# Kernel optimization log

Hardware: AMD Instinct MI355X
Metric: run time of the kernel (lower is better)

The kernel has to match this reference:

```python
import jax, jax.numpy as jnp
import numpy as np

DIM = 1024
NH = 16        # query heads
NKV = 4        # kv heads
HD = 64        # head dim
GROUPS = NH // NKV
SPATIAL = 16
NZ = SPATIAL * SPATIAL  # 256 latent tokens with 2D structure
SOFT_CAP = 50.0
SCALE = HD ** -0.5
EPS = 1e-6


def rope_2d_cos_sin(nz, hd, spatial, dtype):
    # 2D RoPE: first half of head_dim encodes row position, second half column.
    pos = jnp.arange(nz)
    row = (pos // spatial).astype(jnp.float32)
    col = (pos % spatial).astype(jnp.float32)
    quarter = hd // 4
    inv_freq = 1.0 / (10000.0 ** (jnp.arange(quarter, dtype=jnp.float32) / quarter))
    f_row = row[:, None] * inv_freq[None, :]   # (nz, hd/4)
    f_col = col[:, None] * inv_freq[None, :]   # (nz, hd/4)
    emb = jnp.concatenate([f_row, f_col], axis=-1)      # (nz, hd/2)
    emb = jnp.concatenate([emb, emb], axis=-1)          # (nz, hd)
    return jnp.cos(emb).astype(dtype), jnp.sin(emb).astype(dtype)


def rotate_half(x):
    x1, x2 = jnp.split(x, 2, axis=-1)
    return jnp.concatenate([-x2, x1], axis=-1)


def apply_rotary(x, cos, sin):
    return x * cos + rotate_half(x) * sin


def rms_norm(x, w):
    # RMSNorm over head_dim with learned per-dim scale (QKNorm)
    return x * jax.lax.rsqrt(jnp.mean(x * x, axis=-1, keepdims=True) + EPS) * w


def setup_inputs() -> dict:
    key = jax.random.key(0)
    ks = jax.random.split(key, 7)
    B, T, S = 4, 16, 264
    x = jax.random.normal(ks[0], (B, T, S, DIM), dtype=jnp.float32)
    wq = jax.random.normal(ks[1], (NH * HD, DIM), dtype=jnp.float32) * 0.02
    wk = jax.random.normal(ks[2], (NKV * HD, DIM), dtype=jnp.float32) * 0.02
    wv = jax.random.normal(ks[3], (NKV * HD, DIM), dtype=jnp.float32) * 0.02
    wo = jax.random.normal(ks[4], (DIM, NH * HD), dtype=jnp.float32) * 0.02
    q_norm_w = jnp.ones((HD,), dtype=jnp.float32)
    k_norm_w = jnp.ones((HD,), dtype=jnp.float32)
    return {"x": x, "wq": wq, "wk": wk, "wv": wv, "wo": wo,
            "q_norm_w": q_norm_w, "k_norm_w": k_norm_w}


def reference(x, wq, wk, wv, wo, q_norm_w, k_norm_w):
    B, T, S, D = x.shape
    xf = x.reshape(B * T, S, D)
    # projections (torch Linear: y = x @ W.T)
    q = (xf @ wq.T).reshape(B * T, S, NH, HD).transpose(0, 2, 1, 3)   # (BT,NH,S,HD)
    k = (xf @ wk.T).reshape(B * T, S, NKV, HD).transpose(0, 2, 1, 3)  # (BT,NKV,S,HD)
    v = (xf @ wv.T).reshape(B * T, S, NKV, HD).transpose(0, 2, 1, 3)
    # QKNorm
    q = rms_norm(q, q_norm_w)
    k = rms_norm(k, k_norm_w)
    # partial 2D RoPE on latent tokens only
    cos, sin = rope_2d_cos_sin(NZ, HD, SPATIAL, q.dtype)
    cos = cos[None, None]  # (1,1,NZ,HD)
    sin = sin[None, None]
    q = jnp.concatenate([apply_rotary(q[:, :, :NZ], cos, sin), q[:, :, NZ:]], axis=2)
    k = jnp.concatenate([apply_rotary(k[:, :, :NZ], cos, sin), k[:, :, NZ:]], axis=2)
    # GQA: expand kv heads (repeat_interleave == jnp.repeat)
    k = jnp.repeat(k, GROUPS, axis=1)
    v = jnp.repeat(v, GROUPS, axis=1)
    # attention with soft cap
    attn = jnp.einsum("bhqd,bhkd->bhqk", q, k) * SCALE
    attn = SOFT_CAP * jnp.tanh(attn / SOFT_CAP)
    attn = jax.nn.softmax(attn, axis=-1)
    out = jnp.einsum("bhqk,bhkd->bhqd", attn, v)
    out = out.transpose(0, 2, 1, 3).reshape(B * T, S, NH * HD)
    out = out @ wo.T
    return out.reshape(B, T, S, D)
```

## Files before the change

### kernel.cpp

```cpp
#include <hip/hip_runtime.h>

typedef __bf16 bf16;
typedef __bf16 bf16x8 __attribute__((ext_vector_type(8)));
typedef float  f32x4  __attribute__((ext_vector_type(4)));

#define DIM   1024
#define NH    16
#define NKV   4
#define HD    64
#define SLEN  264
#define BTOT  64
#define MROWS (BTOT * SLEN)
#define NQKV  1536
#define NZ    256
#define VPAD  288

__device__ __forceinline__ void gl_lds16(const bf16* g, bf16* l) {
    __builtin_amdgcn_global_load_lds((__attribute__((address_space(1))) void*)(g),
                                     (__attribute__((address_space(3))) void*)(l),
                                     16, 0, 0);
}

__global__ void cvt_f32_bf16(const float* __restrict__ src, bf16* __restrict__ dst, int n) {
    int i = (blockIdx.x * 256 + threadIdx.x) * 4;
    if (i < n) {
        float4 v = *(const float4*)(src + i);
        dst[i + 0] = (bf16)v.x; dst[i + 1] = (bf16)v.y;
        dst[i + 2] = (bf16)v.z; dst[i + 3] = (bf16)v.w;
    }
}

__global__ void cvt_wcat(const float* __restrict__ wq, const float* __restrict__ wk,
                         const float* __restrict__ wv, bf16* __restrict__ dst) {
    int i = (blockIdx.x * 256 + threadIdx.x) * 4;
    const float* src; int off;
    if (i < 1024 * 1024)      { src = wq; off = i; }
    else if (i < 1280 * 1024) { src = wk; off = i - 1024 * 1024; }
    else                      { src = wv; off = i - 1280 * 1024; }
    float4 v = *(const float4*)(src + off);
    dst[i + 0] = (bf16)v.x; dst[i + 1] = (bf16)v.y;
    dst[i + 2] = (bf16)v.z; dst[i + 3] = (bf16)v.w;
}

__global__ void rope_tab_kernel(float2* __restrict__ ctab) {
    int i = blockIdx.x * 256 + threadIdx.x;
    int s = i >> 5, d = i & 31;
    const float LN1 = 0.5756462732485115f;
    float pos = (d < 16) ? (float)(s >> 4) : (float)(s & 15);
    float ang = pos * expf(-(float)(d & 15) * LN1);
    float sn, cs; sincosf(ang, &sn, &cs);
    ctab[i] = make_float2(cs, sn);
}


#define GATE4  asm volatile("s_waitcnt vmcnt(4)" ::: "memory")
#define NOGATE do {} while (0)

#define STAGE_A(DST, H, KT) do {                                                       \
    gl_lds16(Ag + (size_t)((H) * 128 + ars[0]) * DIM + (KT) * 64 + acs[0] * 8,         \
             (DST) + (wid * 64) * 8);                                                  \
    gl_lds16(Ag + (size_t)((H) * 128 + ars[1]) * DIM + (KT) * 64 + acs[1] * 8,         \
             (DST) + (512 + wid * 64) * 8);                                            \
} while (0)

#define STAGE_B(DST, KS, KT) do {                                                      \
    gl_lds16(Bg + (size_t)brs[0] * DIM + (KT) * 64 + (KS) * 32 + bcs[0] * 8,           \
             (DST) + (wid * 64) * 8);                                                  \
    gl_lds16(Bg + (size_t)brs[1] * DIM + (KT) * 64 + (KS) * 32 + bcs[1] * 8,           \
             (DST) + (512 + wid * 64) * 8);                                            \
} while (0)

#define PHASE(AARR, BARR, AA, KS, STAGE_STMT, GATE_STMT) do {                          \
    const bf16* Ab_ = (AARR) + aRdBase + axor[KS];                                     \
    const bf16* Bb_ = (BARR) + bRdBase + bxorv;                                        \
    bf16x8 af_[4], bf_[4];                                                             \
    _Pragma("unroll")                                                                  \
    for (int i_ = 0; i_ < 4; i_++) af_[i_] = *(const bf16x8*)(Ab_ + i_ * 1024);        \
    _Pragma("unroll")                                                                  \
    for (int n_ = 0; n_ < 4; n_++) bf_[n_] = *(const bf16x8*)(Bb_ + n_ * 512);         \
    STAGE_STMT;                                                                        \
    GATE_STMT;                                                                         \
    asm volatile("s_barrier" ::: "memory");                                            \
    __builtin_amdgcn_s_setprio(1);                                                     \
    _Pragma("unroll")                                                                  \
    for (int i_ = 0; i_ < 4; i_++)                                                     \
        _Pragma("unroll")                                                              \
        for (int n_ = 0; n_ < 4; n_++)                                                 \
            acc[AA][i_][n_] = __builtin_amdgcn_mfma_f32_16x16x32_bf16(                 \
                af_[i_], bf_[n_], acc[AA][i_][n_], 0, 0, 0);                           \
    __builtin_amdgcn_s_setprio(0);                                                     \
    asm volatile("s_barrier" ::: "memory");                                            \
} while (0)

__device__ __forceinline__ void gemm256_core(const bf16* __restrict__ Ag,
                                             const bf16* __restrict__ Bg,
                                             f32x4 (&acc)[2][4][4]) {
    __shared__ __align__(16) bf16 A00[128 * 64], A01[128 * 64], A10[128 * 64], A11[128 * 64];
    __shared__ __align__(16) bf16 B00[256 * 32], B01[256 * 32], B10[256 * 32], B11[256 * 32];

    const int tid  = threadIdx.x;
    const int wid  = tid >> 6, lane = tid & 63;
    const int quad = lane >> 4, r16 = lane & 15;
    const int wm = wid & 1, wn = wid >> 1;

    int ars[2], acs[2], brs[2], bcs[2];
#pragma unroll
    for (int k = 0; k < 2; k++) {
        int s = k * 512 + tid;
        ars[k] = s >> 3; acs[k] = (s & 7) ^ (ars[k] & 7);
        brs[k] = s >> 2; bcs[k] = (s & 3) ^ (brs[k] & 3);
    }
    const int aRdBase = (wm * 64 + r16) * 64;
    const int bRdBase = (wn * 64 + r16) * 32;
    const int axor[2] = { (quad ^ (r16 & 7)) * 8, ((4 + quad) ^ (r16 & 7)) * 8 };
    const int bxorv   = (quad ^ (r16 & 3)) * 8;

    STAGE_A(A00, 0, 0); STAGE_A(A01, 1, 0);
    STAGE_B(B00, 0, 0); STAGE_B(B01, 1, 0);
    STAGE_A(A10, 0, 1); STAGE_B(B10, 0, 1);
    GATE4;
    asm volatile("s_barrier" ::: "memory");

#pragma unroll 1
    for (int it = 0; it < 8; ++it) {
        const int t1 = 2 * it + 1;
        int t2 = 2 * it + 2; if (t2 > 15) t2 = 15;
        int t3 = 2 * it + 3; if (t3 > 15) t3 = 15;
        PHASE(A00, B00, 0, 0, STAGE_A(A11, 1, t1), NOGATE);
        PHASE(A00, B01, 0, 1, STAGE_B(B11, 1, t1), NOGATE);
        PHASE(A01, B00, 1, 0, STAGE_A(A00, 0, t2), NOGATE);
        PHASE(A01, B01, 1, 1, STAGE_B(B00, 0, t2), GATE4);
        PHASE(A10, B10, 0, 0, STAGE_A(A01, 1, t2), NOGATE);
        PHASE(A10, B11, 0, 1, STAGE_B(B01, 1, t2), NOGATE);
        PHASE(A11, B10, 1, 0, STAGE_A(A10, 0, t3), NOGATE);
        PHASE(A11, B11, 1, 1, STAGE_B(B10, 0, t3), GATE4);
    }
}

__device__ __forceinline__ int xcd_swizzle(int orig, int nwg) {
    int q = nwg >> 3, r = nwg & 7;
    int xcd = orig & 7, lid = orig >> 3;
    return (xcd < r ? xcd * (q + 1) : r * (q + 1) + (xcd - r) * q) + lid;
}

__global__ __launch_bounds__(512) void gemm_qkv(const bf16* __restrict__ A,
                                                const bf16* __restrict__ Bw,
                                                bf16* __restrict__ out,
                                                const float* __restrict__ qw,
                                                const float* __restrict__ kw,
                                                const float2* __restrict__ ctab) {
    const int nwg = (MROWS / 256) * (NQKV / 256);
    int wg = xcd_swizzle(blockIdx.x, nwg);
    const int bm = wg / 6, bn = wg - bm * 6;

    f32x4 acc[2][4][4];
#pragma unroll
    for (int a = 0; a < 2; a++)
#pragma unroll
        for (int i = 0; i < 4; i++)
#pragma unroll
            for (int n = 0; n < 4; n++) acc[a][i][n] = (f32x4){0.f, 0.f, 0.f, 0.f};

    gemm256_core(A + (size_t)bm * 256 * DIM, Bw + (size_t)bn * 256 * DIM, acc);

    const int tid  = threadIdx.x;
    const int wid  = tid >> 6, lane = tid & 63;
    const int quad = lane >> 4, r16 = lane & 15;
    const int wm = wid & 1, wn = wid >> 1;
    const int colbase = bn * 256 + wn * 64;
    const int rowb    = bm * 256 + wm * 64;

    if (bn < 5) {
        const float* w = (bn < 4) ? qw : kw;
        float wreg[4];
#pragma unroll
        for (int n = 0; n < 4; n++) wreg[n] = w[n * 16 + r16];
#pragma unroll
        for (int a = 0; a < 2; a++)
#pragma unroll
            for (int i = 0; i < 4; i++)
#pragma unroll
                for (int r = 0; r < 4; r++) {
                    float ss = 0.f;
#pragma unroll
                    for (int n = 0; n < 4; n++) ss += acc[a][i][n][r] * acc[a][i][n][r];
                    ss += __shfl_xor(ss, 1, 64);
                    ss += __shfl_xor(ss, 2, 64);
                    ss += __shfl_xor(ss, 4, 64);
                    ss += __shfl_xor(ss, 8, 64);
                    float rms = rsqrtf(ss * (1.f / 64.f) + 1e-6f);
                    float xv[4];
#pragma unroll
                    for (int n = 0; n < 4; n++) xv[n] = acc[a][i][n][r] * rms * wreg[n];
                    int gm = rowb + a * 128 + i * 16 + quad * 4 + r;
                    int s = gm % SLEN;
                    if (s < NZ) {
                        float2 cs0 = ctab[s * 32 + r16];
                        float2 cs1 = ctab[s * 32 + 16 + r16];
                        float a0 = xv[0] * cs0.x - xv[2] * cs0.y;
                        float a2 = xv[2] * cs0.x + xv[0] * cs0.y;
                        float a1 = xv[1] * cs1.x - xv[3] * cs1.y;
                        float a3 = xv[3] * cs1.x + xv[1] * cs1.y;
                        xv[0] = a0; xv[1] = a1; xv[2] = a2; xv[3] = a3;
                    }
                    size_t rowoff = (size_t)gm * NQKV + colbase + r16;
#pragma unroll
                    for (int n = 0; n < 4; n++) out[rowoff + n * 16] = (bf16)xv[n];
                }
    } else {
#pragma unroll
        for (int a = 0; a < 2; a++)
#pragma unroll
            for (int i = 0; i < 4; i++)
#pragma unroll
                for (int r = 0; r < 4; r++) {
                    int gm = rowb + a * 128 + i * 16 + quad * 4 + r;
                    size_t rowoff = (size_t)gm * NQKV + colbase + r16;
#pragma unroll
                    for (int n = 0; n < 4; n++) out[rowoff + n * 16] = (bf16)acc[a][i][n][r];
                }
    }
}

__global__ __launch_bounds__(512) void gemm_bt(const bf16* __restrict__ A,
                                               const bf16* __restrict__ Bw,
                                               float* __restrict__ Cout) {
    const int nwg = (MROWS / 256) * (DIM / 256);
    int wg = xcd_swizzle(blockIdx.x, nwg);
    const int bm = wg / 4, bn = wg - bm * 4;

    f32x4 acc[2][4][4];
#pragma unroll
    for (int a = 0; a < 2; a++)
#pragma unroll
        for (int i = 0; i < 4; i++)
#pragma unroll
            for (int n = 0; n < 4; n++) acc[a][i][n] = (f32x4){0.f, 0.f, 0.f, 0.f};

    gemm256_core(A + (size_t)bm * 256 * DIM, Bw + (size_t)bn * 256 * DIM, acc);

    const int tid  = threadIdx.x;
    const int wid  = tid >> 6, lane = tid & 63;
    const int quad = lane >> 4, r16 = lane & 15;
    const int wm = wid & 1, wn = wid >> 1;
    const int colbase = bn * 256 + wn * 64;
    const int rowb    = bm * 256 + wm * 64;
#pragma unroll
    for (int a = 0; a < 2; a++)
#pragma unroll
        for (int i = 0; i < 4; i++)
#pragma unroll
            for (int r = 0; r < 4; r++) {
                int gm = rowb + a * 128 + i * 16 + quad * 4 + r;
                size_t rowoff = (size_t)gm * DIM + colbase + r16;
#pragma unroll
                for (int n = 0; n < 4; n++) Cout[rowoff + n * 16] = acc[a][i][n][r];
            }
}

__global__ __launch_bounds__(256) void vtrans_kernel(const bf16* __restrict__ qkv,
                                                     bf16* __restrict__ vt) {
    __shared__ bf16 Ls[64 * 272];
    const int tid = threadIdx.x;
    const int b = blockIdx.x, bt = b >> 2, kv = b & 3;
    const int part = tid >> 5;
    const int rr   = tid & 31;
#pragma unroll
    for (int pass = 0; pass < 9; ++pass) {
        int row = pass * 32 + rr;
        if (row < SLEN) {
            bf16x8 v = *(const bf16x8*)(qkv + (size_t)(bt * SLEN + row) * NQKV + 1280 + kv * 64 + part * 8);
#pragma unroll
            for (int j = 0; j < 8; j++) Ls[(part * 8 + j) * 272 + row] = v[j];
        }
    }
    __syncthreads();
    const int d = tid >> 2, seg = tid & 3;
    size_t obase = ((size_t)b * 64 + d) * VPAD;
#pragma unroll
    for (int m = 0; m < 9; ++m) {
        int col = seg * 72 + m * 8;
        bf16x8 o;
#pragma unroll
        for (int j = 0; j < 8; j++) {
            int s = col + j;
            o[j] = (s < SLEN) ? Ls[d * 272 + s] : (bf16)0.f;
        }
        *(bf16x8*)(vt + obase + col) = o;
    }
}

__global__ __launch_bounds__(256) void attn_kernel(const bf16* __restrict__ qkv,
                                                   const bf16* __restrict__ vt,
                                                   bf16* __restrict__ aout) {
    const int PLD = 40;
    __shared__ __align__(16) bf16 Pb[4][2][16 * PLD];

    const int tid = threadIdx.x;
    const int wid = tid >> 6, lane = tid & 63;
    const int quad = lane >> 4, r16 = lane & 15;
    const int qp = blockIdx.x;
    const int kv = blockIdx.y, bt = blockIdx.z;
    const int h = kv * 4 + wid;

    bf16x8 qa[2][2];
#pragma unroll
    for (int qi = 0; qi < 2; qi++) {
        int q0 = qp * 32 + qi * 16 + r16;
        int qcl = q0 < SLEN ? q0 : SLEN - 1;
        const bf16* qb = qkv + (size_t)(bt * SLEN + qcl) * NQKV + h * HD + quad * 8;
        qa[qi][0] = *(const bf16x8*)qb;
        qa[qi][1] = *(const bf16x8*)(qb + 32);
    }

    f32x4 oacc[2][4];
    float lsum[2][4];
#pragma unroll
    for (int qi = 0; qi < 2; qi++)
#pragma unroll
        for (int i = 0; i < 4; i++) { oacc[qi][i] = (f32x4){0.f, 0.f, 0.f, 0.f}; lsum[qi][i] = 0.f; }

    const bf16* kbase = qkv + (size_t)bt * SLEN * NQKV + 1024 + kv * HD + quad * 8;
    const bf16* vbase = vt + (size_t)(bt * 4 + kv) * HD * VPAD;

    bf16x8 nk[2][2];
#pragma unroll
    for (int kt = 0; kt < 2; kt++) {
        int key = kt * 16 + r16;
        const bf16* kp = kbase + (size_t)key * NQKV;
        nk[kt][0] = *(const bf16x8*)kp;
        nk[kt][1] = *(const bf16x8*)(kp + 32);
    }

    for (int c = 0; c < 9; ++c) {
        bf16x8 ck[2][2];
#pragma unroll
        for (int kt = 0; kt < 2; kt++) { ck[kt][0] = nk[kt][0]; ck[kt][1] = nk[kt][1]; }
        if (c < 8) {
#pragma unroll
            for (int kt = 0; kt < 2; kt++) {
                int key = (c + 1) * 32 + kt * 16 + r16;
                int kc = key < SLEN ? key : SLEN - 1;
                const bf16* kp = kbase + (size_t)kc * NQKV;
                nk[kt][0] = *(const bf16x8*)kp;
                nk[kt][1] = *(const bf16x8*)(kp + 32);
            }
        }
        bf16x8 cv[4];
#pragma unroll
        for (int dt = 0; dt < 4; ++dt)
            cv[dt] = *(const bf16x8*)(vbase + (size_t)(dt * 16 + r16) * VPAD + c * 32 + quad * 8);

        f32x4 s[2][2];
#pragma unroll
        for (int qi = 0; qi < 2; qi++)
#pragma unroll
            for (int kt = 0; kt < 2; kt++) {
                f32x4 t = (f32x4){0.f, 0.f, 0.f, 0.f};
                t = __builtin_amdgcn_mfma_f32_16x16x32_bf16(qa[qi][0], ck[kt][0], t, 0, 0, 0);
                t = __builtin_amdgcn_mfma_f32_16x16x32_bf16(qa[qi][1], ck[kt][1], t, 0, 0, 0);
                s[qi][kt] = t;
            }

#pragma unroll
        for (int qi = 0; qi < 2; qi++) {
            bf16* Pw = &Pb[wid][qi][0];
#pragma unroll
            for (int kt = 0; kt < 2; kt++)
#pragma unroll
                for (int r = 0; r < 4; ++r) {
                    int key = c * 32 + kt * 16 + r16;
                    float sc = s[qi][kt][r];
                    float z = sc * 0.0025f;
                    float z2 = z * z;
                    float poly = fmaf(z2, fmaf(z2, 0.133333333f, -0.333333333f), 1.f);
                    float p = exp2f(sc * 0.18033688f * poly);
                    p = (key < SLEN) ? p : 0.f;
                    bf16 pb = (bf16)p;
                    lsum[qi][r] += (float)pb;
                    Pw[(quad * 4 + r) * PLD + kt * 16 + r16] = pb;
                }
            bf16x8 pa = *(const bf16x8*)&Pw[r16 * PLD + quad * 8];
#pragma unroll
            for (int dt = 0; dt < 4; ++dt)
                oacc[qi][dt] = __builtin_amdgcn_mfma_f32_16x16x32_bf16(pa, cv[dt], oacc[qi][dt], 0, 0, 0);
        }
    }

#pragma unroll
    for (int qi = 0; qi < 2; qi++)
#pragma unroll
        for (int r = 0; r < 4; ++r) {
            float l = lsum[qi][r];
            l += __shfl_xor(l, 1, 64);
            l += __shfl_xor(l, 2, 64);
            l += __shfl_xor(l, 4, 64);
            l += __shfl_xor(l, 8, 64);
            float inv = 1.f / l;
            int q = qp * 32 + qi * 16 + quad * 4 + r;
            if (q < SLEN) {
                size_t base = (size_t)(bt * SLEN + q) * (NH * HD) + h * HD;
#pragma unroll
                for (int dt = 0; dt < 4; ++dt)
                    aout[base + dt * 16 + r16] = (bf16)(oacc[qi][dt][r] * inv);
            }
        }
}

extern "C" void kernel_launch(void* const* d_in, const int* in_sizes, int n_in,
                              void* d_out, int out_size, void* d_ws, size_t ws_size,
                              hipStream_t stream) {
    const float* x   = (const float*)d_in[0];
    const float* wq  = (const float*)d_in[1];
    const float* wk  = (const float*)d_in[2];
    const float* wv  = (const float*)d_in[3];
    const float* wo  = (const float*)d_in[4];
    const float* qnw = (const float*)d_in[5];
    const float* knw = (const float*)d_in[6];

    bf16* xbf  = (bf16*)d_ws;
    bf16* wcat = xbf  + (size_t)MROWS * DIM;
    bf16* wobf = wcat + (size_t)NQKV * DIM;
    bf16* qkv  = wobf + (size_t)DIM * DIM;
    bf16* vt   = qkv  + (size_t)MROWS * NQKV;
    float2* ctab = (float2*)(vt + (size_t)BTOT * NKV * HD * VPAD);
    bf16* aout = xbf;

    rope_tab_kernel<<<32, 256, 0, stream>>>(ctab);
    cvt_f32_bf16<<<(MROWS * DIM) / 1024, 256, 0, stream>>>(x, xbf, MROWS * DIM);
    cvt_wcat<<<(NQKV * DIM) / 1024, 256, 0, stream>>>(wq, wk, wv, wcat);
    cvt_f32_bf16<<<(DIM * DIM) / 1024, 256, 0, stream>>>(wo, wobf, DIM * DIM);

    gemm_qkv<<<(MROWS / 256) * (NQKV / 256), 512, 0, stream>>>(xbf, wcat, qkv, qnw, knw, ctab);
    vtrans_kernel<<<BTOT * NKV, 256, 0, stream>>>(qkv, vt);
    attn_kernel<<<dim3(9, NKV, BTOT), 256, 0, stream>>>(qkv, vt, aout);
    gemm_bt<<<(MROWS / 256) * (DIM / 256), 512, 0, stream>>>(aout, wobf, (float*)d_out);
}
```

Before: 372.0 us.

## Restructure QKV GEMM main loop to 32-wide K steps with double-buffered LDS

Rewrites the 256x256 GEMM core so each K step covers 32 columns instead of 64. The shared-memory layout becomes two A and two B buffers with a pair-row XOR swizzle, and the loop runs 16 iterations of 4 phases, each with finer-grained vmcnt(1) gating. Explicit lgkmcnt waits and sched_barriers are added so MFMA issue follows the LDS reads. The aim is finer overlap of global-to-LDS staging with MFMA work and smaller LDS use, at the cost of more barriers per unit of K.

```diff
diff --git a/kernel.cpp b/kernel.cpp
--- a/kernel.cpp
+++ b/kernel.cpp
@@ -52,95 +52,97 @@
     ctab[i] = make_float2(cs, sn);
 }
 
-
-#define GATE4  asm volatile("s_waitcnt vmcnt(4)" ::: "memory")
+__device__ __forceinline__ int xcd_swizzle(int orig, int nwg) {
+    int q = nwg >> 3, r = nwg & 7;
+    int xcd = orig & 7, lid = orig >> 3;
+    return (xcd < r ? xcd * (q + 1) : r * (q + 1) + (xcd - r) * q) + lid;
+}
+
+
+#define GATE1  asm volatile("s_waitcnt vmcnt(1)" ::: "memory")
 #define NOGATE do {} while (0)
 
-#define STAGE_A(DST, H, KT) do {                                                       \
-    gl_lds16(Ag + (size_t)((H) * 128 + ars[0]) * DIM + (KT) * 64 + acs[0] * 8,         \
-             (DST) + (wid * 64) * 8);                                                  \
-    gl_lds16(Ag + (size_t)((H) * 128 + ars[1]) * DIM + (KT) * 64 + acs[1] * 8,         \
-             (DST) + (512 + wid * 64) * 8);                                            \
-} while (0)
-
-#define STAGE_B(DST, KS, KT) do {                                                      \
-    gl_lds16(Bg + (size_t)brs[0] * DIM + (KT) * 64 + (KS) * 32 + bcs[0] * 8,           \
-             (DST) + (wid * 64) * 8);                                                  \
-    gl_lds16(Bg + (size_t)brs[1] * DIM + (KT) * 64 + (KS) * 32 + bcs[1] * 8,           \
-             (DST) + (512 + wid * 64) * 8);                                            \
-} while (0)
-
-#define PHASE(AARR, BARR, AA, KS, STAGE_STMT, GATE_STMT) do {                          \
-    const bf16* Ab_ = (AARR) + aRdBase + axor[KS];                                     \
-    const bf16* Bb_ = (BARR) + bRdBase + bxorv;                                        \
-    bf16x8 af_[4], bf_[4];                                                             \
-    _Pragma("unroll")                                                                  \
-    for (int i_ = 0; i_ < 4; i_++) af_[i_] = *(const bf16x8*)(Ab_ + i_ * 1024);        \
-    _Pragma("unroll")                                                                  \
-    for (int n_ = 0; n_ < 4; n_++) bf_[n_] = *(const bf16x8*)(Bb_ + n_ * 512);         \
-    STAGE_STMT;                                                                        \
-    GATE_STMT;                                                                         \
-    asm volatile("s_barrier" ::: "memory");                                            \
-    __builtin_amdgcn_s_setprio(1);                                                     \
-    _Pragma("unroll")                                                                  \
-    for (int i_ = 0; i_ < 4; i_++)                                                     \
-        _Pragma("unroll")                                                              \
-        for (int n_ = 0; n_ < 4; n_++)                                                 \
-            acc[AA][i_][n_] = __builtin_amdgcn_mfma_f32_16x16x32_bf16(                 \
-                af_[i_], bf_[n_], acc[AA][i_][n_], 0, 0, 0);                           \
-    __builtin_amdgcn_s_setprio(0);                                                     \
-    asm volatile("s_barrier" ::: "memory");                                            \
+#define STA(DBUF, SITE, KT) gl_lds16(Asrc[SITE] + (KT) * 32, (DBUF) + (SITE) * 4096 + wid * 512)
+#define STB(DBUF, SITE, KT) gl_lds16(Bsrc[SITE] + (KT) * 32, (DBUF) + (SITE) * 4096 + wid * 512)
+
+#define PHASE(Ad, Bd, AA, GATE_STMT, ...) do {                                 \
+    bf16x8 af_[4], bf_[4];                                                     \
+    _Pragma("unroll")                                                          \
+    for (int i_ = 0; i_ < 4; i_++) {                                           \
+        af_[i_] = *(const bf16x8*)((Ad) + aOff[AA][i_]);                       \
+        bf_[i_] = *(const bf16x8*)((Bd) + bOff[i_]);                           \
+    }                                                                          \
+    __VA_ARGS__;                                                               \
+    GATE_STMT;                                                                 \
+    __builtin_amdgcn_s_barrier();                                              \
+    asm volatile("s_waitcnt lgkmcnt(0)" ::: "memory");                         \
+    __builtin_amdgcn_sched_barrier(0);                                         \
+    __builtin_amdgcn_s_setprio(1);                                             \
+    _Pragma("unroll")                                                          \
+    for (int i_ = 0; i_ < 4; i_++)                                             \
+        _Pragma("unroll")                                                      \
+        for (int n_ = 0; n_ < 4; n_++)                                         \
+            acc[AA][i_][n_] = __builtin_amdgcn_mfma_f32_16x16x32_bf16(         \
+                af_[i_], bf_[n_], acc[AA][i_][n_], 0, 0, 0);                   \
+    __builtin_amdgcn_s_setprio(0);                                             \
+    __builtin_amdgcn_s_barrier();                                              \
 } while (0)
 
 __device__ __forceinline__ void gemm256_core(const bf16* __restrict__ Ag,
                                              const bf16* __restrict__ Bg,
                                              f32x4 (&acc)[2][4][4]) {
-    __shared__ __align__(16) bf16 A00[128 * 64], A01[128 * 64], A10[128 * 64], A11[128 * 64];
-    __shared__ __align__(16) bf16 B00[256 * 32], B01[256 * 32], B10[256 * 32], B11[256 * 32];
+    __shared__ __align__(16) bf16 A0[8192], A1[8192], B0[8192], B1[8192];
 
     const int tid  = threadIdx.x;
     const int wid  = tid >> 6, lane = tid & 63;
     const int quad = lane >> 4, r16 = lane & 15;
     const int wm = wid & 1, wn = wid >> 1;
 
-    int ars[2], acs[2], brs[2], bcs[2];
-#pragma unroll
-    for (int k = 0; k < 2; k++) {
-        int s = k * 512 + tid;
-        ars[k] = s >> 3; acs[k] = (s & 7) ^ (ars[k] & 7);
-        brs[k] = s >> 2; bcs[k] = (s & 3) ^ (brs[k] & 3);
-    }
-    const int aRdBase = (wm * 64 + r16) * 64;
-    const int bRdBase = (wn * 64 + r16) * 32;
-    const int axor[2] = { (quad ^ (r16 & 7)) * 8, ((4 + quad) ^ (r16 & 7)) * 8 };
-    const int bxorv   = (quad ^ (r16 & 3)) * 8;
-
-    STAGE_A(A00, 0, 0); STAGE_A(A01, 1, 0);
-    STAGE_B(B00, 0, 0); STAGE_B(B01, 1, 0);
-    STAGE_A(A10, 0, 1); STAGE_B(B10, 0, 1);
-    GATE4;
-    asm volatile("s_barrier" ::: "memory");
+    const bf16* Asrc[2]; const bf16* Bsrc[2];
+#pragma unroll
+    for (int s = 0; s < 2; s++) {
+        int p  = s * 64 + wid * 8 + (lane >> 3);
+        int sl = (lane & 7) ^ (p & 7);
+        int R  = (p << 1) | (sl >> 2);
+        int kc = sl & 3;
+        Asrc[s] = Ag + (size_t)R * DIM + kc * 8;
+        Bsrc[s] = Bg + (size_t)R * DIM + kc * 8;
+    }
+
+    int aOff[2][4], bOff[4];
+#pragma unroll
+    for (int a = 0; a < 2; a++)
+#pragma unroll
+        for (int i = 0; i < 4; i++) {
+            int R = a * 128 + wm * 64 + i * 16 + r16;
+            int p = R >> 1;
+            int sp = (((R & 1) * 4 + quad) ^ (p & 7));
+            aOff[a][i] = p * 64 + sp * 8;
+        }
+#pragma unroll
+    for (int n = 0; n < 4; n++) {
+        int R = wn * 64 + n * 16 + r16;
+        int p = R >> 1;
+        int sp = (((R & 1) * 4 + quad) ^ (p & 7));
+        bOff[n] = p * 64 + sp * 8;
+    }
+
+    STA(A0, 0, 0); STA(A0, 1, 0);
+    STB(B0, 0, 0); STB(B0, 1, 0);
+    STA(A1, 0, 1);
+    GATE1;
+    __builtin_amdgcn_s_barrier();
 
 #pragma unroll 1
-    for (int it = 0; it < 8; ++it) {
-        const int t1 = 2 * it + 1;
-        int t2 = 2 * it + 2; if (t2 > 15) t2 = 15;
-        int t3 = 2 * it + 3; if (t3 > 15) t3 = 15;
-        PHASE(A00, B00, 0, 0, STAGE_A(A11, 1, t1), NOGATE);
-        PHASE(A00, B01, 0, 1, STAGE_B(B11, 1, t1), NOGATE);
-        PHASE(A01, B00, 1, 0, STAGE_A(A00, 0, t2), NOGATE);
-        PHASE(A01, B01, 1, 1, STAGE_B(B00, 0, t2), GATE4);
-        PHASE(A10, B10, 0, 0, STAGE_A(A01, 1, t2), NOGATE);
-        PHASE(A10, B11, 0, 1, STAGE_B(B01, 1, t2), NOGATE);
-        PHASE(A11, B10, 1, 0, STAGE_A(A10, 0, t3), NOGATE);
-        PHASE(A11, B11, 1, 1, STAGE_B(B10, 0, t3), GATE4);
-    }
-}
-
-__device__ __forceinline__ int xcd_swizzle(int orig, int nwg) {
-    int q = nwg >> 3, r = nwg & 7;
-    int xcd = orig & 7, lid = orig >> 3;
-    return (xcd < r ? xcd * (q + 1) : r * (q + 1) + (xcd - r) * q) + lid;
+    for (int it = 0; it < 16; ++it) {
+        const int u1 = 2 * it + 1;
+        int u2 = 2 * it + 2; if (u2 > 31) u2 = 31;
+        int u3 = 2 * it + 3; if (u3 > 31) u3 = 31;
+        PHASE(A0, B0, 0, NOGATE, STA(A1, 1, u1), STB(B1, 0, u1));
+        PHASE(A0, B0, 1, GATE1,  STB(B1, 1, u1), STA(A0, 0, u2));
+        PHASE(A1, B1, 0, NOGATE, STA(A0, 1, u2), STB(B0, 0, u2));
+        PHASE(A1, B1, 1, GATE1,  STB(B0, 1, u2), STA(A1, 0, u3));
+    }
 }
 
 __global__ __launch_bounds__(512) void gemm_qkv(const bf16* __restrict__ A,
```

New measurement: 423.4 us. 13.8% more time.
